# Performance work log

Hardware: AMD Instinct MI355X
Metric: run time of the kernel (lower is better)

## Reference

```python
import jax, jax.numpy as jnp
import numpy as np

N_HEADS, DK, DV, G = 12, 64, 64, 1
W_WIN, R_RAND = 3, 2
B, S, D = 2, 2048, 768


def _make_idx_tensor(seq_len, g, w, r, seed=0):
    # Mirrors SparseMultiHeadAttention.create_idx_tensor: each middle row is
    # [0] + r random key indices + w consecutive window key indices.
    rng = np.random.default_rng(seed)
    s2 = seq_len - 2 * g
    shift = max(g - (w - 1) // 2, 0)
    windows = np.arange(s2)[:, None] + np.arange(w)[None, :] + shift  # (s2, w)
    rand = np.empty((s2, r), np.int64)
    half = (w - 1) // 2
    for i in range(s2):
        pos = i + g
        cand = rng.choice(np.arange(1, seq_len), size=r + w + 2, replace=False)
        cand = cand[np.abs(cand - pos) > half][:r]
        rand[i] = cand
    idx = np.concatenate([np.zeros((s2, 1), np.int64), rand, windows], axis=1)
    return jnp.asarray(idx)  # (s2, 1+r+w)


def setup_inputs() -> dict:
    key = jax.random.key(0)
    ks = jax.random.split(key, 7)
    scale = 0.02  # keep projected logits in a sane range for softmax
    return {
        "Q": jax.random.normal(ks[0], (B, S, D), jnp.float32),
        "K": jax.random.normal(ks[1], (B, S, D), jnp.float32),
        "V": jax.random.normal(ks[2], (B, S, D), jnp.float32),
        "Wq": jax.random.normal(ks[3], (N_HEADS * DK, D), jnp.float32) * scale,
        "Wk": jax.random.normal(ks[4], (N_HEADS * DK, D), jnp.float32) * scale,
        "Wv": jax.random.normal(ks[5], (N_HEADS * DV, D), jnp.float32) * scale,
        "Wo": jax.random.normal(ks[6], (D, N_HEADS * DV), jnp.float32) * scale,
        "idx_tensor": _make_idx_tensor(S, G, W_WIN, R_RAND),
    }


def reference(Q, K, V, Wq, Wk, Wv, Wo, idx_tensor):
    b, s, d = Q.shape
    h, dk, dv, g = N_HEADS, DK, DV, G
    # projections (torch Linear: x @ W.T), split heads -> (b, h, s, d_head)
    q = (Q @ Wq.T).reshape(b, s, h, dk).transpose(0, 2, 1, 3)
    k = (K @ Wk.T).reshape(b, s, h, dk).transpose(0, 2, 1, 3)
    v = (V @ Wv.T).reshape(b, s, h, dv).transpose(0, 2, 1, 3)

    # global rows (first g, last g) attend densely over all keys
    gidx = jnp.concatenate([jnp.arange(g), jnp.arange(s - g, s)])
    global_attn = jnp.einsum('bhgd,bhtd->bhgt', q[:, :, gidx, :], k)  # (b,h,2g,s)

    # middle rows: gather [first, random..., window...] keys per row
    comb = k[:, :, idx_tensor, :]                    # (b, h, s2, 1+r+w, dk)
    scores = jnp.einsum('bhsd,bhskd->bhsk', q[:, :, g:s - g, :], comb)

    # scatter into a dense (s, s) score matrix (zeros elsewhere), as the source does
    result = jnp.zeros((b, h, s, s), q.dtype)
    result = result.at[:, :, gidx, :].set(global_attn)
    rows = jnp.arange(g, s - g)[:, None]             # (s2, 1)
    result = result.at[:, :, rows, idx_tensor].set(scores)
    result = result / jnp.sqrt(jnp.asarray(dk, q.dtype))

    attn = jax.nn.softmax(result, axis=-1)
    out = jnp.einsum('bhst,bhtd->bhsd', attn, v)     # (b, h, s, dv)
    out = out.transpose(0, 2, 1, 3).reshape(b, s, h * dv)
    return out @ Wo.T
```

## Files before the change

### kernel.cpp

```cpp
#include <hip/hip_runtime.h>
#include <hip/hip_bf16.h>

#define S_LEN   2048
#define D_MODEL 768
#define NH      12
#define HD      64
#define NI      6
#define S2      2046
#define BB      2
#define NCH     8
#define CHK     256
#define SPB     (S2 / 2)

typedef unsigned short ushort_t;
typedef __attribute__((ext_vector_type(8))) short short8v;
typedef __attribute__((ext_vector_type(4))) float f32x4;

__device__ __forceinline__ unsigned short bf16_rne(float x) {
    union { float f; unsigned int u; } c; c.f = x;
    unsigned int u = c.u + 0x7fffu + ((c.u >> 16) & 1u);
    return (unsigned short)(u >> 16);
}
__device__ __forceinline__ float bf16_f(unsigned short h) {
    union { unsigned int u; float f; } c; c.u = ((unsigned int)h) << 16;
    return c.f;
}

__device__ __forceinline__ void gload16(const ushort_t* g, ushort_t* l) {
    __builtin_amdgcn_global_load_lds(
        (const __attribute__((address_space(1))) void*)g,
        (__attribute__((address_space(3))) void*)l, 16, 0, 0);
}

struct CvtAll {
    const float* Q; const float* K; const float* V;
    const float* Wq; const float* Wk; const float* Wv; const float* Wo;
    ushort_t* Qc; ushort_t* Kc; ushort_t* Vc;
    ushort_t* Wqc; ushort_t* Wkc; ushort_t* Wvc; ushort_t* Woc;
    float* vs;
};

__global__ __launch_bounds__(256) void cvt_all(CvtAll a) {
    const int z = blockIdx.z;
    const int tid = threadIdx.x;
    if (z == 4) {
        if (blockIdx.x == 0)
            for (int i = tid; i < BB * D_MODEL; i += 256) a.vs[i] = 0.f;
        return;
    }
    const float* s; ushort_t* d; long i;
    if (z < 3) {
        s = (z == 0) ? a.Q : (z == 1) ? a.K : a.V;
        d = (z == 0) ? a.Qc : (z == 1) ? a.Kc : a.Vc;
        i = ((long)blockIdx.x * 256 + tid) * 8;
    } else {
        const long WSZ = (long)D_MODEL * D_MODEL;
        long f = ((long)blockIdx.x * 256 + tid) * 8;
        if (f >= 4 * WSZ) return;
        const int which = (int)(f / WSZ);
        i = f % WSZ;
        s = (which == 0) ? a.Wq : (which == 1) ? a.Wk : (which == 2) ? a.Wv : a.Wo;
        d = (which == 0) ? a.Wqc : (which == 1) ? a.Wkc : (which == 2) ? a.Wvc : a.Woc;
    }
    float4 v0 = *(const float4*)&s[i];
    float4 v1 = *(const float4*)&s[i + 4];
    short8v o;
    o[0] = (short)bf16_rne(v0.x); o[1] = (short)bf16_rne(v0.y);
    o[2] = (short)bf16_rne(v0.z); o[3] = (short)bf16_rne(v0.w);
    o[4] = (short)bf16_rne(v1.x); o[5] = (short)bf16_rne(v1.y);
    o[6] = (short)bf16_rne(v1.z); o[7] = (short)bf16_rne(v1.w);
    *(short8v*)&d[i] = o;
}

struct GemmArgs { const ushort_t* A; const ushort_t* W; ushort_t* C; float* Cf; float* vs; };

constexpr int GK = 768, GN = 768, GBK = 32, GNT = GK / GBK;
constexpr int GX = 6, GY = 32;

__global__ __launch_bounds__(256) void bf16_gemm_nt(GemmArgs g0, GemmArgs g1, GemmArgs g2) {
    const int nwg = GX * GY * gridDim.z;
    int flat = (blockIdx.z * GY + blockIdx.y) * GX + blockIdx.x;
    flat = (flat & 7) * (nwg >> 3) + (flat >> 3);
    const int bz = flat / (GX * GY);
    const int rem = flat - bz * (GX * GY);
    const int by = rem / GX;
    const int bx = rem - by * GX;

    GemmArgs g = (bz == 0) ? g0 : ((bz == 1) ? g1 : g2);

    __shared__ ushort_t As[3][4096];
    __shared__ ushort_t Bs[3][4096];

    const int tid  = threadIdx.x;
    const int lane = tid & 63;
    const int w    = tid >> 6;
    const int wm   = w & 1;
    const int wn   = w >> 1;
    const int bm   = by * 128;
    const int bn   = bx * 128;
    const int fr   = lane & 15;
    const int blkr = lane >> 4;

    f32x4 acc[4][4];
    #pragma unroll
    for (int i = 0; i < 4; ++i)
        #pragma unroll
        for (int j = 0; j < 4; ++j)
            acc[i][j] = (f32x4){0.f, 0.f, 0.f, 0.f};

    const int row0 = tid >> 2;
    const int row1 = row0 + 64;
    const int blk0 = (tid & 3) ^ ((row0 >> 1) & 3);
    const int blk1 = (tid & 3) ^ ((row1 >> 1) & 3);
    const ushort_t* Ag0 = g.A + (size_t)(bm + row0) * GK + blk0 * 8;
    const ushort_t* Ag1 = g.A + (size_t)(bm + row1) * GK + blk1 * 8;
    const ushort_t* Bg0 = g.W + (size_t)(bn + row0) * GK + blk0 * 8;
    const ushort_t* Bg1 = g.W + (size_t)(bn + row1) * GK + blk1 * 8;
    const int l0 = w * 512;
    const int l1 = 2048 + w * 512;

    int aoff[4], boff[4];
    #pragma unroll
    for (int i = 0; i < 4; ++i) {
        const int ra = wm * 64 + i * 16 + fr;
        aoff[i] = (ra * 4 + (blkr ^ ((ra >> 1) & 3))) * 8;
        const int rb = wn * 64 + i * 16 + fr;
        boff[i] = (rb * 4 + (blkr ^ ((rb >> 1) & 3))) * 8;
    }

    gload16(Ag0, &As[0][l0]); gload16(Ag1, &As[0][l1]);
    gload16(Bg0, &Bs[0][l0]); gload16(Bg1, &Bs[0][l1]);
    gload16(Ag0 + GBK, &As[1][l0]); gload16(Ag1 + GBK, &As[1][l1]);
    gload16(Bg0 + GBK, &Bs[1][l0]); gload16(Bg1 + GBK, &Bs[1][l1]);

    for (int t = 0; t < GNT; ++t) {
        if (t < GNT - 1) asm volatile("s_waitcnt vmcnt(4)" ::: "memory");
        else             asm volatile("s_waitcnt vmcnt(0)" ::: "memory");
        __builtin_amdgcn_s_barrier();

        if (t + 2 < GNT) {
            const int ko = (t + 2) * GBK;
            const int nb = (t + 2) % 3;
            gload16(Ag0 + ko, &As[nb][l0]); gload16(Ag1 + ko, &As[nb][l1]);
            gload16(Bg0 + ko, &Bs[nb][l0]); gload16(Bg1 + ko, &Bs[nb][l1]);
        }

        const ushort_t* as = As[t % 3];
        const ushort_t* bs = Bs[t % 3];
        short8v a[4], b[4];
        #pragma unroll
        for (int i = 0; i < 4; ++i) a[i] = *(const short8v*)&as[aoff[i]];
        #pragma unroll
        for (int i = 0; i < 4; ++i) b[i] = *(const short8v*)&bs[boff[i]];
        #pragma unroll
        for (int i = 0; i < 4; ++i)
            #pragma unroll
            for (int j = 0; j < 4; ++j)
                acc[i][j] = __builtin_amdgcn_mfma_f32_16x16x32_bf16(a[i], b[j], acc[i][j], 0, 0, 0);
    }

    const int crow0 = bm + wm * 64 + ((lane >> 4) << 2);
    const int ccol0 = bn + wn * 64 + fr;
    if (g.Cf) {
        #pragma unroll
        for (int i = 0; i < 4; ++i)
            #pragma unroll
            for (int j = 0; j < 4; ++j)
                #pragma unroll
                for (int r = 0; r < 4; ++r)
                    g.Cf[(size_t)(crow0 + i * 16 + r) * GN + ccol0 + j * 16] = acc[i][j][r];
    } else {
        #pragma unroll
        for (int i = 0; i < 4; ++i)
            #pragma unroll
            for (int j = 0; j < 4; ++j)
                #pragma unroll
                for (int r = 0; r < 4; ++r)
                    g.C[(size_t)(crow0 + i * 16 + r) * GN + ccol0 + j * 16] = bf16_rne(acc[i][j][r]);
        if (g.vs) {
            const int bsel = (bm >= S_LEN) ? 1 : 0;
            #pragma unroll
            for (int j = 0; j < 4; ++j) {
                float part = 0.f;
                #pragma unroll
                for (int i = 0; i < 4; ++i)
                    #pragma unroll
                    for (int r = 0; r < 4; ++r)
                        part += bf16_f(bf16_rne(acc[i][j][r]));
                atomicAdd(&g.vs[bsel * D_MODEL + ccol0 + j * 16], part);
            }
        }
    }
}

__global__ __launch_bounds__(768) void attn_fused(
    const ushort_t* __restrict__ q, const ushort_t* __restrict__ k, const ushort_t* __restrict__ v,
    const float* __restrict__ vsum, const int* __restrict__ idx,
    float* __restrict__ part, ushort_t* __restrict__ ao) {
    const int bid = blockIdx.x;
    const int tid = threadIdx.x;

    __shared__ float qs[HD];
    __shared__ float ps[CHK];
    __shared__ float red[8];
    __shared__ float redv[96][72];

    if (bid < SPB * BB) {
        const int b = bid & 1;
        const int i0 = (bid >> 1) * 2;
        const int c = tid;

        int id[2][NI];
        #pragma unroll
        for (int r = 0; r < 2; ++r)
            #pragma unroll
            for (int j = 0; j < NI; ++j) id[r][j] = idx[(i0 + r) * NI + j];
        bool dup[2][NI];
        #pragma unroll
        for (int r = 0; r < 2; ++r)
            #pragma unroll
            for (int j = 0; j < NI; ++j) {
                bool d = false;
                #pragma unroll
                for (int j2 = 0; j2 < NI; ++j2)
                    if (j2 < j) d = d || (id[r][j2] == id[r][j]);
                dup[r][j] = d;
            }

        const size_t rb0 = ((size_t)(b * S_LEN + i0 + 1)) * D_MODEL + c;
        const float qv0 = bf16_f(q[rb0]);
        const float qv1 = bf16_f(q[rb0 + D_MODEL]);

        float kv[2][NI], vv[2][NI];
        #pragma unroll
        for (int r = 0; r < 2; ++r)
            #pragma unroll
            for (int j = 0; j < NI; ++j) {
                const size_t kb = ((size_t)(b * S_LEN + id[r][j])) * D_MODEL + c;
                kv[r][j] = bf16_f(k[kb]);
                vv[r][j] = bf16_f(v[kb]);
            }

        float p[2][NI];
        #pragma unroll
        for (int j = 0; j < NI; ++j) { p[0][j] = qv0 * kv[0][j]; p[1][j] = qv1 * kv[1][j]; }

        #pragma unroll
        for (int off = 32; off; off >>= 1) {
            #pragma unroll
            for (int r = 0; r < 2; ++r)
                #pragma unroll
                for (int j = 0; j < NI; ++j) p[r][j] += __shfl_xor(p[r][j], off);
        }

        const float vsc = vsum[b * D_MODEL + c];
        #pragma unroll
        for (int r = 0; r < 2; ++r) {
            float acc = vsc;
            float Z = 0.f;
            int u = 0;
            #pragma unroll
            for (int j = 0; j < NI; ++j) {
                if (dup[r][j]) continue;
                float e = expf(p[r][j] * 0.125f);
                Z += e;
                u += 1;
                acc += (e - 1.f) * vv[r][j];
            }
            Z += (float)(S_LEN - u);
            ao[rb0 + (size_t)r * D_MODEL] = bf16_rne(acc / Z);
        }
        return;
    }

    const int pid = bid - SPB * BB;
    const int ch = pid & 7;
    const int rowsel = (pid >> 3) & 1;
    const int hb = pid >> 4;
    const int h = hb % NH;
    const int b = hb / NH;
    const int row = rowsel ? (S_LEN - 1) : 0;

    if (tid < HD) qs[tid] = bf16_f(q[((size_t)(b * S_LEN + row)) * D_MODEL + h * HD + tid]);
    __syncthreads();

    float s = 0.f;
    if (tid < CHK) {
        const int t = ch * CHK + tid;
        const ushort_t* kp = &k[((size_t)(b * S_LEN + t)) * D_MODEL + h * HD];
        #pragma unroll
        for (int dd = 0; dd < 8; ++dd) {
            short8v kk = *(const short8v*)&kp[dd * 8];
            #pragma unroll
            for (int e = 0; e < 8; ++e)
                s += qs[dd * 8 + e] * bf16_f((unsigned short)kk[e]);
        }
        s *= 0.125f;
    }

    float m = s;
    #pragma unroll
    for (int off = 32; off; off >>= 1) m = fmaxf(m, __shfl_xor(m, off));
    if (tid < CHK && (tid & 63) == 0) red[tid >> 6] = m;
    __syncthreads();
    m = fmaxf(fmaxf(red[0], red[1]), fmaxf(red[2], red[3]));

    float e = (tid < CHK) ? expf(s - m) : 0.f;
    if (tid < CHK) ps[tid] = e;
    float zp = e;
    #pragma unroll
    for (int off = 32; off; off >>= 1) zp += __shfl_xor(zp, off);
    if (tid < CHK && (tid & 63) == 0) red[4 + (tid >> 6)] = zp;
    __syncthreads();
    const float E = red[4] + red[5] + red[6] + red[7];

    const int g8 = tid >> 3;
    const int d8 = (tid & 7) * 8;
    float a8[8] = {};
    for (int tt = g8; tt < CHK; tt += 96) {
        const float wgt = ps[tt];
        short8v v8 = *(const short8v*)&v[((size_t)(b * S_LEN + ch * CHK + tt)) * D_MODEL + h * HD + d8];
        #pragma unroll
        for (int e2 = 0; e2 < 8; ++e2)
            a8[e2] += wgt * bf16_f((unsigned short)v8[e2]);
    }
    #pragma unroll
    for (int e2 = 0; e2 < 8; ++e2) redv[g8][d8 + e2] = a8[e2];
    __syncthreads();
    if (tid < HD) {
        float o = 0.f;
        #pragma unroll
        for (int gg = 0; gg < 96; ++gg) o += redv[gg][tid];
        float* pr = part + ((size_t)((hb * 2 + rowsel) * NCH + ch)) * (HD + 2);
        pr[2 + tid] = o;
        if (tid == 0) { pr[0] = m; pr[1] = E; }
    }
}

__global__ __launch_bounds__(64) void global_attn_fin(
    const float* __restrict__ part, ushort_t* __restrict__ ao) {
    const int rb = blockIdx.x;
    const int rowsel = rb & 1;
    const int hb = rb >> 1;
    const int h = hb % NH;
    const int b = hb / NH;
    const int row = rowsel ? (S_LEN - 1) : 0;
    const int d = threadIdx.x;

    const float* pr = part + (size_t)rb * NCH * (HD + 2);
    float M = -1e30f;
    #pragma unroll
    for (int c = 0; c < NCH; ++c) M = fmaxf(M, pr[c * (HD + 2)]);
    float Z = 0.f, acc = 0.f;
    #pragma unroll
    for (int c = 0; c < NCH; ++c) {
        float wgt = expf(pr[c * (HD + 2)] - M);
        Z   += pr[c * (HD + 2) + 1] * wgt;
        acc += pr[c * (HD + 2) + 2 + d] * wgt;
    }
    ao[((size_t)(b * S_LEN + row)) * D_MODEL + h * HD + d] = bf16_rne(acc / Z);
}

extern "C" void kernel_launch(void* const* d_in, const int* in_sizes, int n_in,
                              void* d_out, int out_size, void* d_ws, size_t ws_size,
                              hipStream_t stream) {
    const float* Q  = (const float*)d_in[0];
    const float* K  = (const float*)d_in[1];
    const float* V  = (const float*)d_in[2];
    const float* Wq = (const float*)d_in[3];
    const float* Wk = (const float*)d_in[4];
    const float* Wv = (const float*)d_in[5];
    const float* Wo = (const float*)d_in[6];
    const int*  idx = (const int*)d_in[7];
    float* out = (float*)d_out;

    const size_t SZ  = (size_t)BB * S_LEN * D_MODEL;
    const size_t WSZ = (size_t)D_MODEL * D_MODEL;

    ushort_t* Qc  = (ushort_t*)d_ws;
    ushort_t* Kc  = Qc  + SZ;
    ushort_t* Vc  = Kc  + SZ;
    ushort_t* Wqc = Vc  + SZ;
    ushort_t* Wkc = Wqc + WSZ;
    ushort_t* Wvc = Wkc + WSZ;
    ushort_t* Woc = Wvc + WSZ;
    ushort_t* qb  = Woc + WSZ;
    ushort_t* kb  = qb  + SZ;
    ushort_t* vb  = kb  + SZ;
    ushort_t* ao  = vb  + SZ;
    float* vs   = (float*)(ao + SZ);
    float* part = vs + BB * D_MODEL;

    {
        CvtAll a{Q, K, V, Wq, Wk, Wv, Wo, Qc, Kc, Vc, Wqc, Wkc, Wvc, Woc, vs};
        cvt_all<<<dim3((unsigned)(SZ / 2048), 1, 5), 256, 0, stream>>>(a);
    }
    {
        GemmArgs g0{Qc, Wqc, qb, nullptr, nullptr};
        GemmArgs g1{Kc, Wkc, kb, nullptr, nullptr};
        GemmArgs g2{Vc, Wvc, vb, nullptr, vs};
        bf16_gemm_nt<<<dim3(GX, GY, 3), 256, 0, stream>>>(g0, g1, g2);
    }
    attn_fused<<<dim3(SPB * BB + NCH * 2 * NH * BB), 768, 0, stream>>>(
        qb, kb, vb, vs, idx, part, ao);
    global_attn_fin<<<dim3(2 * NH * BB), 64, 0, stream>>>(part, ao);
    {
        GemmArgs g{ao, Woc, nullptr, out, nullptr};
        bf16_gemm_nt<<<dim3(GX, GY, 1), 256, 0, stream>>>(g, g, g);
    }
}
```

Before: 192.6 us.

## Widen GEMM K-tile to 64 and switch to double-buffered LDS pipeline

The projection GEMM now loads 64-wide K slices instead of 32, with a new 8-way XOR swizzle for the LDS layout. The triple-buffered pipeline with explicit vmcnt waits is replaced by two buffers separated by __syncthreads. This halves the number of K iterations and barriers and doubles the MFMA work per iteration. In exchange, prefetch depth drops to one tile and a full barrier waits on every outstanding load, so latency hiding may get worse.

```diff
diff --git a/kernel.cpp b/kernel.cpp
--- a/kernel.cpp
+++ b/kernel.cpp
@@ -74,7 +74,7 @@
 
 struct GemmArgs { const ushort_t* A; const ushort_t* W; ushort_t* C; float* Cf; float* vs; };
 
-constexpr int GK = 768, GN = 768, GBK = 32, GNT = GK / GBK;
+constexpr int GK = 768, GN = 768, GBK = 64, GNT = GK / GBK;
 constexpr int GX = 6, GY = 32;
 
 __global__ __launch_bounds__(256) void bf16_gemm_nt(GemmArgs g0, GemmArgs g1, GemmArgs g2) {
@@ -88,8 +88,8 @@
 
     GemmArgs g = (bz == 0) ? g0 : ((bz == 1) ? g1 : g2);
 
-    __shared__ ushort_t As[3][4096];
-    __shared__ ushort_t Bs[3][4096];
+    __shared__ ushort_t As[2][8192];
+    __shared__ ushort_t Bs[2][8192];
 
     const int tid  = threadIdx.x;
     const int lane = tid & 63;
@@ -108,55 +108,64 @@
         for (int j = 0; j < 4; ++j)
             acc[i][j] = (f32x4){0.f, 0.f, 0.f, 0.f};
 
-    const int row0 = tid >> 2;
-    const int row1 = row0 + 64;
-    const int blk0 = (tid & 3) ^ ((row0 >> 1) & 3);
-    const int blk1 = (tid & 3) ^ ((row1 >> 1) & 3);
-    const ushort_t* Ag0 = g.A + (size_t)(bm + row0) * GK + blk0 * 8;
-    const ushort_t* Ag1 = g.A + (size_t)(bm + row1) * GK + blk1 * 8;
-    const ushort_t* Bg0 = g.W + (size_t)(bn + row0) * GK + blk0 * 8;
-    const ushort_t* Bg1 = g.W + (size_t)(bn + row1) * GK + blk1 * 8;
-    const int l0 = w * 512;
-    const int l1 = 2048 + w * 512;
-
-    int aoff[4], boff[4];
+    const int srow    = w * 32 + (lane >> 3);
+    const int src_blk = (lane & 7) ^ (lane >> 3);
+    const ushort_t* Agp[4];
+    const ushort_t* Bgp[4];
+    #pragma unroll
+    for (int r = 0; r < 4; ++r) {
+        Agp[r] = g.A + (size_t)(bm + srow + r * 8) * GK + src_blk * 8;
+        Bgp[r] = g.W + (size_t)(bn + srow + r * 8) * GK + src_blk * 8;
+    }
+    const int ldst = w * 2048;
+
+    int aoff[4][2], boff[4][2];
     #pragma unroll
     for (int i = 0; i < 4; ++i) {
         const int ra = wm * 64 + i * 16 + fr;
-        aoff[i] = (ra * 4 + (blkr ^ ((ra >> 1) & 3))) * 8;
         const int rb = wn * 64 + i * 16 + fr;
-        boff[i] = (rb * 4 + (blkr ^ ((rb >> 1) & 3))) * 8;
-    }
-
-    gload16(Ag0, &As[0][l0]); gload16(Ag1, &As[0][l1]);
-    gload16(Bg0, &Bs[0][l0]); gload16(Bg1, &Bs[0][l1]);
-    gload16(Ag0 + GBK, &As[1][l0]); gload16(Ag1 + GBK, &As[1][l1]);
-    gload16(Bg0 + GBK, &Bs[1][l0]); gload16(Bg1 + GBK, &Bs[1][l1]);
+        #pragma unroll
+        for (int kk = 0; kk < 2; ++kk) {
+            aoff[i][kk] = ra * 64 + (((kk << 2) | blkr) ^ (ra & 7)) * 8;
+            boff[i][kk] = rb * 64 + (((kk << 2) | blkr) ^ (rb & 7)) * 8;
+        }
+    }
+
+    #pragma unroll
+    for (int r = 0; r < 4; ++r) {
+        gload16(Agp[r], &As[0][ldst + r * 512]);
+        gload16(Bgp[r], &Bs[0][ldst + r * 512]);
+    }
+    __syncthreads();
 
     for (int t = 0; t < GNT; ++t) {
-        if (t < GNT - 1) asm volatile("s_waitcnt vmcnt(4)" ::: "memory");
-        else             asm volatile("s_waitcnt vmcnt(0)" ::: "memory");
-        __builtin_amdgcn_s_barrier();
-
-        if (t + 2 < GNT) {
-            const int ko = (t + 2) * GBK;
-            const int nb = (t + 2) % 3;
-            gload16(Ag0 + ko, &As[nb][l0]); gload16(Ag1 + ko, &As[nb][l1]);
-            gload16(Bg0 + ko, &Bs[nb][l0]); gload16(Bg1 + ko, &Bs[nb][l1]);
-        }
-
-        const ushort_t* as = As[t % 3];
-        const ushort_t* bs = Bs[t % 3];
-        short8v a[4], b[4];
-        #pragma unroll
-        for (int i = 0; i < 4; ++i) a[i] = *(const short8v*)&as[aoff[i]];
-        #pragma unroll
-        for (int i = 0; i < 4; ++i) b[i] = *(const short8v*)&bs[boff[i]];
+        const int cur = t & 1;
+        if (t + 1 < GNT) {
+            const int ko = (t + 1) * GBK;
+            #pragma unroll
+            for (int r = 0; r < 4; ++r) {
+                gload16(Agp[r] + ko, &As[cur ^ 1][ldst + r * 512]);
+                gload16(Bgp[r] + ko, &Bs[cur ^ 1][ldst + r * 512]);
+            }
+        }
+        const ushort_t* as = As[cur];
+        const ushort_t* bs = Bs[cur];
+        short8v a[4][2], b[4][2];
+        #pragma unroll
+        for (int i = 0; i < 4; ++i) {
+            a[i][0] = *(const short8v*)&as[aoff[i][0]];
+            a[i][1] = *(const short8v*)&as[aoff[i][1]];
+            b[i][0] = *(const short8v*)&bs[boff[i][0]];
+            b[i][1] = *(const short8v*)&bs[boff[i][1]];
+        }
         #pragma unroll
         for (int i = 0; i < 4; ++i)
             #pragma unroll
-            for (int j = 0; j < 4; ++j)
-                acc[i][j] = __builtin_amdgcn_mfma_f32_16x16x32_bf16(a[i], b[j], acc[i][j], 0, 0, 0);
+            for (int j = 0; j < 4; ++j) {
+                acc[i][j] = __builtin_amdgcn_mfma_f32_16x16x32_bf16(a[i][0], b[j][0], acc[i][j], 0, 0, 0);
+                acc[i][j] = __builtin_amdgcn_mfma_f32_16x16x32_bf16(a[i][1], b[j][1], acc[i][j], 0, 0, 0);
+            }
+        __syncthreads();
     }
 
     const int crow0 = bm + wm * 64 + ((lane >> 4) << 2);
```

Measured after the change: 199.1 us. 3.4% more time.
